# Kernel tuning notes

Hardware: AMD Instinct MI355X
Metric: run time of the kernel (lower is better)

## Reference

```python
import jax, jax.numpy as jnp
import numpy as np

NUM_HEADS = 16
NUM_KV_HEADS = 4
ROPE_THETA = 10000.0


def apply_rope(x, position_ids, theta):
    # x: [B, S, h, d]; position_ids: [B, S]
    d = x.shape[-1]
    freqs = 1.0 / theta ** (jnp.arange(0, d, 2, dtype=jnp.float32) / d)  # [d/2]
    angles = position_ids.astype(jnp.float32)[..., None] * freqs          # [B, S, d/2]
    cos = jnp.cos(angles)[:, :, None, :]                                  # [B, S, 1, d/2]
    sin = jnp.sin(angles)[:, :, None, :]
    xr = x.astype(jnp.float32).reshape(*x.shape[:-1], d // 2, 2)
    x0, x1 = xr[..., 0], xr[..., 1]
    o0 = x0 * cos - x1 * sin
    o1 = x0 * sin + x1 * cos
    out = jnp.stack((o0, o1), axis=-1).reshape(*x.shape)
    return out.astype(x.dtype)


def setup_inputs() -> dict:
    key = jax.random.key(0)
    k0, k1, k2, k3, k4 = jax.random.split(key, 5)
    B, S, H = 1, 2048, 2048
    Hkv = H // (NUM_HEADS // NUM_KV_HEADS)  # 512
    init_scale = 0.02 / np.sqrt(H)
    return {
        "hidden_states": jax.random.normal(k0, (B, S, H), jnp.float32),
        "attention_mask": jnp.ones((B, S), jnp.int32),
        "segment_ids": jnp.zeros((B, S), jnp.int32),
        "position_ids": jnp.broadcast_to(jnp.arange(S, dtype=jnp.int32)[None], (B, S)),
        "Wq": jax.random.normal(k1, (H, H), jnp.float32) * init_scale,
        "Wk": jax.random.normal(k2, (H, Hkv), jnp.float32) * init_scale,
        "Wv": jax.random.normal(k3, (H, Hkv), jnp.float32) * init_scale,
        "Wo": jax.random.normal(k4, (H, H), jnp.float32) * init_scale,
    }


def reference(hidden_states, attention_mask, segment_ids, position_ids, Wq, Wk, Wv, Wo):
    B, S, H = hidden_states.shape
    nh, nkv = NUM_HEADS, NUM_KV_HEADS
    g = nh // nkv
    hd = H // nh

    xq = (hidden_states @ Wq).reshape(B, S, nh, hd)
    xk = (hidden_states @ Wk).reshape(B, S, nkv, hd)
    xv = (hidden_states @ Wv).reshape(B, S, nkv, hd)
    # GQA repeat: 'b s (h d) -> b s (h g) d' == repeat each kv head g times contiguously
    xk = jnp.repeat(xk, g, axis=2)  # [B, S, nh, hd]
    xv = jnp.repeat(xv, g, axis=2)

    xq = apply_rope(xq, position_ids, ROPE_THETA)
    xk = apply_rope(xk, position_ids, ROPE_THETA)

    # masks: causal AND padding AND segment
    causal = jnp.tril(jnp.ones((S, S), dtype=bool))[None, None]            # [1,1,S,S]
    pad = (attention_mask > 0)[:, None, None, :]                            # [B,1,1,S]
    seg = (segment_ids[:, :, None] == segment_ids[:, None, :])[:, None]     # [B,1,S,S]
    mask = causal & pad & seg                                               # [B,1,S,S]

    scale = 1.0 / np.sqrt(hd)
    logits = jnp.einsum("bqhd,bkhd->bhqk", xq.astype(jnp.float32), xk.astype(jnp.float32)) * scale
    logits = jnp.where(mask, logits, jnp.finfo(jnp.float32).min)
    probs = jax.nn.softmax(logits, axis=-1).astype(xv.dtype)
    attn = jnp.einsum("bhqk,bkhd->bqhd", probs, xv)                         # [B,S,nh,hd]

    out = attn.reshape(B, S, H) @ Wo
    return out
```

## Files before the change

### kernel.cpp

```cpp
#include <hip/hip_runtime.h>
#include <hip/hip_bf16.h>
#include <stdint.h>
#include <math.h>

#define SS 2048
#define HH 2048
#define NH 16
#define NKV 4
#define HD 128
#define HKV 512
#define NQKV 3072

typedef __bf16 bf16x8 __attribute__((ext_vector_type(8)));
typedef float f32x4 __attribute__((ext_vector_type(4)));

static_assert(sizeof(bf16x8) == 16, "bf16x8 must be 16B");

__device__ __forceinline__ void async_ld16(const void* gp, void* lp) {
  __builtin_amdgcn_global_load_lds(
      (const __attribute__((address_space(1))) unsigned int*)(uintptr_t)gp,
      (__attribute__((address_space(3))) unsigned int*)(uintptr_t)lp,
      16, 0, 0);
}

__device__ __forceinline__ unsigned short f2bu(float f) {
  __hip_bfloat16 b = __float2bfloat16(f);
  return *reinterpret_cast<unsigned short*>(&b);
}

__global__ __launch_bounds__(256) void k_prep1(
    const float* __restrict__ X, const float* __restrict__ Wq, const float* __restrict__ Wk,
    const float* __restrict__ Wv, const float* __restrict__ Wo,
    const int* __restrict__ amv, const int* __restrict__ seg, int* __restrict__ kseg,
    float2* __restrict__ rtab,
    __hip_bfloat16* __restrict__ Xb, __hip_bfloat16* __restrict__ WqT,
    __hip_bfloat16* __restrict__ WkT, __hip_bfloat16* __restrict__ WvT,
    __hip_bfloat16* __restrict__ WoT) {
  __shared__ __align__(16) __hip_bfloat16 t2[64 * 72];
  int b = blockIdx.x;
  int t = threadIdx.y * 32 + threadIdx.x;
  if (b < 4096) {
    int i = b * 256 + t;
    float4 v = ((const float4*)X)[i];
    ushort4 o;
    o.x = f2bu(v.x); o.y = f2bu(v.y); o.z = f2bu(v.z); o.w = f2bu(v.w);
    ((ushort4*)Xb)[i] = o;
    return;
  }
  b -= 4096;
  if (b >= 2568) {
    int i = (b - 2568) * 256 + t;
    int p = i >> 6, f = i & 63;
    const float L2T_D64 = 0.20762050593046837f;
    float freq = exp2f(-L2T_D64 * (float)f);
    float sn, cs;
    sincosf((float)p * freq, &sn, &cs);
    rtab[i] = make_float2(sn, cs);
    return;
  }
  if (b >= 2560) {
    int i = (b - 2560) * 256 + t;
    kseg[i] = (amv[i] > 0) ? seg[i] : 0x7fffffff;
    return;
  }
  const float* src; __hip_bfloat16* dst; int xtiles;
  if (b < 1024)      { src = Wq; dst = WqT; xtiles = 32; }
  else if (b < 2048) { src = Wo; dst = WoT; xtiles = 32; b -= 1024; }
  else if (b < 2304) { src = Wk; dst = WkT; xtiles = 8;  b -= 2048; }
  else               { src = Wv; dst = WvT; xtiles = 8;  b -= 2304; }
  const int C = xtiles * 64;
  int bx = (b % xtiles) * 64;
  int by = (b / xtiles) * 64;
#pragma unroll
  for (int i = 0; i < 4; i++) {
    int idx = i * 256 + t;
    int r = idx >> 4, c4 = (idx & 15) * 4;
    float4 v = *(const float4*)(src + (size_t)(by + r) * C + bx + c4);
    t2[(c4 + 0) * 72 + r] = __float2bfloat16(v.x);
    t2[(c4 + 1) * 72 + r] = __float2bfloat16(v.y);
    t2[(c4 + 2) * 72 + r] = __float2bfloat16(v.z);
    t2[(c4 + 3) * 72 + r] = __float2bfloat16(v.w);
  }
  __syncthreads();
#pragma unroll
  for (int i = 0; i < 2; i++) {
    int idx = i * 256 + t;
    int rr = idx >> 3, cc = (idx & 7) * 8;
    *(bf16x8*)(dst + (size_t)(bx + rr) * HH + by + cc) =
        *(const bf16x8*)(&t2[rr * 72 + cc]);
  }
}

__global__ __launch_bounds__(256, 2) void k_gemm_qkv(
    const __hip_bfloat16* __restrict__ A, const __hip_bfloat16* __restrict__ B,
    __hip_bfloat16* __restrict__ Qb, __hip_bfloat16* __restrict__ Kb,
    __hip_bfloat16* __restrict__ Vt, const int* __restrict__ pos,
    const float2* __restrict__ rtab) {
  __shared__ __align__(16) __hip_bfloat16 sA0[64 * 64];
  __shared__ __align__(16) __hip_bfloat16 sA1[64 * 64];
  __shared__ __align__(16) __hip_bfloat16 sA2[64 * 64];
  __shared__ __align__(16) __hip_bfloat16 sB0[128 * 64];
  __shared__ __align__(16) __hip_bfloat16 sB1[128 * 64];
  __shared__ __align__(16) __hip_bfloat16 sB2[128 * 64];
  const int tid = threadIdx.x;
  const int lane = tid & 63;
  const int wave = tid >> 6;
  const int bm = blockIdx.y * 64;
  const int bn = blockIdx.x * 128;
  const int wm = (wave & 1) * 32;
  const int wn = (wave >> 1) * 64;
  const int am = lane & 15;
  const int ch = lane >> 4;

  f32x4 acc[2][4] = {};

  auto stage = [&](__hip_bfloat16* sA, __hip_bfloat16* sB, int k0) {
#pragma unroll
    for (int q = 0; q < 2; q++) {
      int c = q * 256 + tid;
      int row = c >> 3, kp = c & 7;
      int col = (kp ^ (row & 7)) * 8;
      async_ld16(A + (size_t)(bm + row) * HH + k0 + col, (char*)sA + c * 16);
    }
#pragma unroll
    for (int q = 0; q < 4; q++) {
      int c = q * 256 + tid;
      int row = c >> 3, kp = c & 7;
      int col = (kp ^ (row & 7)) * 8;
      async_ld16(B + (size_t)(bn + row) * HH + k0 + col, (char*)sB + c * 16);
    }
  };
  auto compute = [&](const __hip_bfloat16* sA, const __hip_bfloat16* sB) {
#pragma unroll
    for (int kb = 0; kb < 2; kb++) {
      bf16x8 a[2], b[4];
#pragma unroll
      for (int i = 0; i < 2; i++) {
        int row = wm + i * 16 + am;
        a[i] = *(const bf16x8*)(sA + row * 64 + (((kb * 4 + ch) ^ (row & 7)) * 8));
      }
#pragma unroll
      for (int j = 0; j < 4; j++) {
        int row = wn + j * 16 + am;
        b[j] = *(const bf16x8*)(sB + row * 64 + (((kb * 4 + ch) ^ (row & 7)) * 8));
      }
#pragma unroll
      for (int i = 0; i < 2; i++)
#pragma unroll
        for (int j = 0; j < 4; j++)
          acc[i][j] = __builtin_amdgcn_mfma_f32_16x16x32_bf16(a[i], b[j], acc[i][j], 0, 0, 0);
    }
  };

  __hip_bfloat16 *cA = sA0, *nA = sA1, *fA = sA2;
  __hip_bfloat16 *cB = sB0, *nB = sB1, *fB = sB2;
  stage(cA, cB, 0);
  stage(nA, nB, 64);
  for (int t = 0; t < 32; ++t) {
    if (t + 1 < 32) asm volatile("s_waitcnt vmcnt(6)" ::: "memory");
    else            asm volatile("s_waitcnt vmcnt(0)" ::: "memory");
    asm volatile("s_barrier" ::: "memory");
    if (t + 2 < 32) stage(fA, fB, (t + 2) * 64);
    compute(cA, cB);
    __hip_bfloat16* tp;
    tp = cA; cA = nA; nA = fA; fA = tp;
    tp = cB; cB = nB; nB = fB; fB = tp;
  }

  const bool isV = (bn >= HH + HKV);
  if (isV) {
#pragma unroll
    for (int j = 0; j < 4; j++) {
      int lc = bn + wn + j * 16 + am - (HH + HKV);
#pragma unroll
      for (int i = 0; i < 2; i++) {
        int row = bm + wm + i * 16 + ch * 4;
        ushort4 o;
        o.x = f2bu(acc[i][j][0]); o.y = f2bu(acc[i][j][1]);
        o.z = f2bu(acc[i][j][2]); o.w = f2bu(acc[i][j][3]);
        *(ushort4*)(Vt + (size_t)lc * SS + row) = o;
      }
    }
  } else {
    const float SCLQ = 0.08838834764831845f * 1.4426950408889634f;
    const bool isQ = (bn < HH);
    int pint[2][4];
#pragma unroll
    for (int i = 0; i < 2; i++)
#pragma unroll
      for (int r = 0; r < 4; r++)
        pint[i][r] = pos[bm + wm + i * 16 + ch * 4 + r];
    const float sgn = (am & 1) ? 1.0f : -1.0f;
#pragma unroll
    for (int j = 0; j < 4; j++) {
      int col = bn + wn + j * 16 + am;
      int lc = isQ ? col : (col - HH);
      int fidx = (lc >> 1) & 63;
#pragma unroll
      for (int i = 0; i < 2; i++)
#pragma unroll
        for (int r = 0; r < 4; r++) {
          float v = acc[i][j][r];
          float px = __shfl_xor(v, 1, 64);
          float2 sc = rtab[pint[i][r] * 64 + fidx];
          float o = v * sc.y + sgn * px * sc.x;
          int row = bm + wm + i * 16 + ch * 4 + r;
          if (isQ) Qb[(size_t)row * HH + col] = __float2bfloat16(o * SCLQ);
          else     Kb[(size_t)row * HKV + lc] = __float2bfloat16(o);
        }
    }
  }
}

__global__ __launch_bounds__(256, 3) void k_gemm_out(
    const __hip_bfloat16* __restrict__ A, const __hip_bfloat16* __restrict__ B,
    float* __restrict__ C) {
  __shared__ __align__(16) __hip_bfloat16 sA0[64 * 64];
  __shared__ __align__(16) __hip_bfloat16 sB0[128 * 64];
  __shared__ __align__(16) __hip_bfloat16 sA1[64 * 64];
  __shared__ __align__(16) __hip_bfloat16 sB1[128 * 64];
  const int tid = threadIdx.x;
  const int lane = tid & 63;
  const int wave = tid >> 6;
  const int bm = blockIdx.y * 64;
  const int bn = blockIdx.x * 128;
  const int wm = (wave & 1) * 32;
  const int wn = (wave >> 1) * 64;
  const int am = lane & 15;
  const int ch = lane >> 4;

  f32x4 acc[2][4] = {};

  auto stage = [&](__hip_bfloat16* sA, __hip_bfloat16* sB, int k0) {
#pragma unroll
    for (int q = 0; q < 2; q++) {
      int c = q * 256 + tid;
      int row = c >> 3, kp = c & 7;
      int col = (kp ^ (row & 7)) * 8;
      async_ld16(A + (size_t)(bm + row) * HH + k0 + col, (char*)sA + c * 16);
    }
#pragma unroll
    for (int q = 0; q < 4; q++) {
      int c = q * 256 + tid;
      int row = c >> 3, kp = c & 7;
      int col = (kp ^ (row & 7)) * 8;
      async_ld16(B + (size_t)(bn + row) * HH + k0 + col, (char*)sB + c * 16);
    }
  };
  auto compute = [&](const __hip_bfloat16* sA, const __hip_bfloat16* sB) {
#pragma unroll
    for (int kb = 0; kb < 2; kb++) {
      bf16x8 a[2], b[4];
#pragma unroll
      for (int i = 0; i < 2; i++) {
        int row = wm + i * 16 + am;
        a[i] = *(const bf16x8*)(sA + row * 64 + (((kb * 4 + ch) ^ (row & 7)) * 8));
      }
#pragma unroll
      for (int j = 0; j < 4; j++) {
        int row = wn + j * 16 + am;
        b[j] = *(const bf16x8*)(sB + row * 64 + (((kb * 4 + ch) ^ (row & 7)) * 8));
      }
#pragma unroll
      for (int i = 0; i < 2; i++)
#pragma unroll
        for (int j = 0; j < 4; j++)
          acc[i][j] = __builtin_amdgcn_mfma_f32_16x16x32_bf16(a[i], b[j], acc[i][j], 0, 0, 0);
    }
  };

  stage(sA0, sB0, 0);
  int k0 = 0;
  while (true) {
    __syncthreads();
    if (k0 + 64 < HH) stage(sA1, sB1, k0 + 64);
    compute(sA0, sB0);
    k0 += 64; if (k0 >= HH) break;
    __syncthreads();
    if (k0 + 64 < HH) stage(sA0, sB0, k0 + 64);
    compute(sA1, sB1);
    k0 += 64; if (k0 >= HH) break;
  }

#pragma unroll
  for (int i = 0; i < 2; i++)
#pragma unroll
    for (int j = 0; j < 4; j++)
#pragma unroll
      for (int r = 0; r < 4; r++) {
        int row = bm + wm + i * 16 + ch * 4 + r;
        int col = bn + wn + j * 16 + am;
        C[(size_t)row * HH + col] = acc[i][j][r];
      }
}

__global__ __launch_bounds__(256, 4) void k_attn(
    const __hip_bfloat16* __restrict__ Qb,
    const __hip_bfloat16* __restrict__ Kb,
    const __hip_bfloat16* __restrict__ Vt,
    const int* __restrict__ seg,
    const int* __restrict__ kseg,
    float* __restrict__ Obuf,
    float* __restrict__ Lbuf) {
  __shared__ __align__(16) __hip_bfloat16 sK[2][32 * 128];
  __shared__ __align__(16) __hip_bfloat16 sV[2][128 * 32];
  __shared__ __align__(16) __hip_bfloat16 sPall[4][16 * 32];

  const int bid = blockIdx.x;
  const int qt = 31 - (bid >> 5);
  const int h = (bid >> 1) & 15;
  const int half = bid & 1;
  const int T = 2 * (qt + 1);
  const int n0 = qt + 1;
  const int kt0 = half ? n0 : 0;
  const int kt1 = half ? T : n0;

  const int kvh = h >> 2;
  const int tid = threadIdx.x, lane = tid & 63, w = tid >> 6;
  const int am = lane & 15, ch = lane >> 4;
  const int qrow0 = qt * 64 + w * 16;
  char* sP = (char*)&sPall[w][0];

  bf16x8 qf[4];
#pragma unroll
  for (int ks = 0; ks < 4; ks++)
    qf[ks] = *(const bf16x8*)(Qb + (size_t)(qrow0 + am) * HH + h * HD + ks * 32 + ch * 8);

  int segq[4];
#pragma unroll
  for (int r = 0; r < 4; r++) segq[r] = seg[qrow0 + ch * 4 + r];
  const int q0 = seg[qrow0];
  const bool quni = __all((segq[0] == q0) && (segq[1] == q0) &&
                          (segq[2] == q0) && (segq[3] == q0));

  f32x4 o_acc[8] = {};
  float l_s[4] = {0.f, 0.f, 0.f, 0.f};

  auto stage = [&](int kt, int p) {
#pragma unroll
    for (int q = 0; q < 2; q++) {
      int c = q * 256 + tid;
      int row = c >> 4, kp = c & 15;
      int col = (kp ^ (row & 15)) * 8;
      async_ld16(Kb + (size_t)(kt * 32 + row) * HKV + kvh * 128 + col, (char*)sK[p] + c * 16);
    }
#pragma unroll
    for (int q = 0; q < 2; q++) {
      int c = q * 256 + tid;
      int row = c >> 2, kp = c & 3;
      int col = (kp ^ ((row >> 1) & 3)) * 8;
      async_ld16(Vt + (size_t)(kvh * 128 + row) * SS + kt * 32 + col, (char*)sV[p] + c * 16);
    }
  };

  stage(kt0, 0);
  for (int kt = kt0; kt < kt1; kt++) {
    const int p = (kt - kt0) & 1;
    const int kbase = kt * 32;
    const bool skip = (kbase > qrow0 + 15);
    __syncthreads();

    int kinfo[2];
    if (!skip) {
#pragma unroll
      for (int jt = 0; jt < 2; jt++) kinfo[jt] = kseg[kbase + jt * 16 + am];
    }
    if (kt + 1 < kt1) stage(kt + 1, p ^ 1);
    if (!skip) {
      f32x4 sacc[2] = {};
      __builtin_amdgcn_s_setprio(1);
#pragma unroll
      for (int ks = 0; ks < 4; ks++)
#pragma unroll
        for (int jt = 0; jt < 2; jt++) {
          bf16x8 kf = *(const bf16x8*)(sK[p] + (jt * 16 + am) * 128 + (((ks * 4 + ch) ^ am) * 8));
          sacc[jt] = __builtin_amdgcn_mfma_f32_16x16x32_bf16(qf[ks], kf, sacc[jt], 0, 0, 0);
        }
      __builtin_amdgcn_s_setprio(0);

      const bool needc = (kbase + 31 > qrow0);
      const bool fast = quni && !needc &&
          __all((kinfo[0] == q0) && (kinfo[1] == q0));

      if (fast) {
#pragma unroll
        for (int jt = 0; jt < 2; jt++)
#pragma unroll
          for (int r = 0; r < 4; r++) {
            float pv = exp2f(sacc[jt][r] - 8.0f);
            l_s[r] += pv;
            int row = ch * 4 + r;
            int chunk = (jt * 2 + (am >> 3)) ^ (row & 3);
            *(__hip_bfloat16*)(sP + row * 64 + chunk * 16 + (am & 7) * 2) =
                __float2bfloat16(pv);
          }
      } else {
#pragma unroll
        for (int jt = 0; jt < 2; jt++) {
          int kk = kbase + jt * 16 + am;
#pragma unroll
          for (int r = 0; r < 4; r++) {
            int qrow = qrow0 + ch * 4 + r;
            bool ok = (kinfo[jt] == segq[r]) && (kk <= qrow);
            float pv = ok ? exp2f(sacc[jt][r] - 8.0f) : 0.0f;
            l_s[r] += pv;
            int row = ch * 4 + r;
            int chunk = (jt * 2 + (am >> 3)) ^ (row & 3);
            *(__hip_bfloat16*)(sP + row * 64 + chunk * 16 + (am & 7) * 2) =
                __float2bfloat16(pv);
          }
        }
      }

      __builtin_amdgcn_s_setprio(1);
      {
        bf16x8 pf = *(const bf16x8*)(sP + am * 64 + ((ch ^ (am & 3)) * 16));
#pragma unroll
        for (int jt = 0; jt < 8; jt++) {
          int vrow = jt * 16 + am;
          bf16x8 vf = *(const bf16x8*)(sV[p] + vrow * 32 + ((ch ^ ((vrow >> 1) & 3)) * 8));
          o_acc[jt] = __builtin_amdgcn_mfma_f32_16x16x32_bf16(pf, vf, o_acc[jt], 0, 0, 0);
        }
      }
      __builtin_amdgcn_s_setprio(0);
    }
  }

#pragma unroll
  for (int off = 1; off < 16; off <<= 1)
#pragma unroll
    for (int r = 0; r < 4; r++) l_s[r] += __shfl_xor(l_s[r], off, 64);
  if (am == 0)
#pragma unroll
    for (int r = 0; r < 4; r++)
      unsafeAtomicAdd(Lbuf + (size_t)(qrow0 + ch * 4 + r) * NH + h, l_s[r]);
#pragma unroll
  for (int jt = 0; jt < 8; jt++)
#pragma unroll
    for (int r = 0; r < 4; r++) {
      int row = qrow0 + ch * 4 + r;
      unsafeAtomicAdd(Obuf + (size_t)row * HH + h * HD + jt * 16 + am, o_acc[jt][r]);
    }
}

__global__ __launch_bounds__(256) void k_norm(
    const float* __restrict__ Obuf, const float* __restrict__ Lbuf,
    __hip_bfloat16* __restrict__ Ab) {
  int i = blockIdx.x * 256 + threadIdx.x;
  int s = i >> 9;
  int hIdx = (i & 511) >> 5;
  float inv = 1.0f / Lbuf[(size_t)s * NH + hIdx];
  float4 v = ((const float4*)Obuf)[i];
  ushort4 o;
  o.x = f2bu(v.x * inv); o.y = f2bu(v.y * inv);
  o.z = f2bu(v.z * inv); o.w = f2bu(v.w * inv);
  ((ushort4*)Ab)[i] = o;
}

extern "C" void kernel_launch(void* const* d_in, const int* in_sizes, int n_in,
                              void* d_out, int out_size, void* d_ws, size_t ws_size,
                              hipStream_t stream) {
  const float* X  = (const float*)d_in[0];
  const int* amv  = (const int*)d_in[1];
  const int* seg  = (const int*)d_in[2];
  const int* pos  = (const int*)d_in[3];
  const float* Wq = (const float*)d_in[4];
  const float* Wk = (const float*)d_in[5];
  const float* Wv = (const float*)d_in[6];
  const float* Wo = (const float*)d_in[7];
  float* out = (float*)d_out;

  char* ws = (char*)d_ws;
  size_t off = 0;
  auto alloc = [&](size_t bytes) { void* p = ws + off; off += (bytes + 255) & ~(size_t)255; return p; };
  __hip_bfloat16* Xb   = (__hip_bfloat16*)alloc((size_t)SS * HH * 2);
  __hip_bfloat16* WqT  = (__hip_bfloat16*)alloc((size_t)HH * HH * 2);
  __hip_bfloat16* WkT  = (__hip_bfloat16*)alloc((size_t)HKV * HH * 2);
  __hip_bfloat16* WvT  = (__hip_bfloat16*)alloc((size_t)HKV * HH * 2);
  __hip_bfloat16* WoT  = (__hip_bfloat16*)alloc((size_t)HH * HH * 2);
  __hip_bfloat16* Qb   = (__hip_bfloat16*)alloc((size_t)SS * HH * 2);
  __hip_bfloat16* Kb   = (__hip_bfloat16*)alloc((size_t)SS * HKV * 2);
  __hip_bfloat16* Vt   = (__hip_bfloat16*)alloc((size_t)HKV * SS * 2);
  __hip_bfloat16* Ab   = (__hip_bfloat16*)alloc((size_t)SS * HH * 2);
  float*          Obuf = (float*)alloc((size_t)SS * HH * 4);
  float*          Lbuf = (float*)alloc((size_t)SS * NH * 4);
  int*            kseg = (int*)alloc((size_t)SS * 4);
  float2*         rtab = (float2*)alloc((size_t)SS * 64 * 8);
  (void)WkT; (void)WvT;

  hipMemsetAsync(Obuf, 0, (size_t)SS * HH * 4 + ((size_t)SS * NH * 4 + 255 & ~(size_t)255), stream);
  k_prep1<<<dim3(7176), dim3(32, 8), 0, stream>>>(X, Wq, Wk, Wv, Wo, amv, seg, kseg, rtab,
                                                  Xb, WqT, WkT, WvT, WoT);
  k_gemm_qkv<<<dim3(NQKV / 128, SS / 64), 256, 0, stream>>>(Xb, WqT, Qb, Kb, Vt, pos, rtab);
  k_attn<<<dim3(1024), 256, 0, stream>>>(Qb, Kb, Vt, seg, kseg, Obuf, Lbuf);
  k_norm<<<dim3(SS * HH / 4 / 256), 256, 0, stream>>>(Obuf, Lbuf, Ab);
  k_gemm_out<<<dim3(HH / 128, SS / 64), 256, 0, stream>>>(Ab, WoT, out);
}
```

Before: 234.0 us.

## Retile QKV GEMM to 128x96 blocks with swizzled 512-block grid and double buffering

Changes the fused QKV projection GEMM from 64x128 tiles over a 24x32 grid to 128x96 tiles over a flat 512-block grid. Block indices are remapped so neighbouring blocks share A/B panels in cache. The triple-buffered async LDS pipeline becomes a double buffer with an extra barrier per iteration. Each wave now computes a 64x48 sub-tile (4x3 MFMA tiles), raising register use and arithmetic per LDS load. The epilogue now decides per 16-column group whether output goes to Q, K, or V, because a 96-wide tile can cross the Q/K/V boundaries.

```diff
diff --git a/kernel.cpp b/kernel.cpp
--- a/kernel.cpp
+++ b/kernel.cpp
@@ -96,108 +96,103 @@
     __hip_bfloat16* __restrict__ Qb, __hip_bfloat16* __restrict__ Kb,
     __hip_bfloat16* __restrict__ Vt, const int* __restrict__ pos,
     const float2* __restrict__ rtab) {
-  __shared__ __align__(16) __hip_bfloat16 sA0[64 * 64];
-  __shared__ __align__(16) __hip_bfloat16 sA1[64 * 64];
-  __shared__ __align__(16) __hip_bfloat16 sA2[64 * 64];
-  __shared__ __align__(16) __hip_bfloat16 sB0[128 * 64];
-  __shared__ __align__(16) __hip_bfloat16 sB1[128 * 64];
-  __shared__ __align__(16) __hip_bfloat16 sB2[128 * 64];
+  __shared__ __align__(16) __hip_bfloat16 sA[2][128 * 64];
+  __shared__ __align__(16) __hip_bfloat16 sB[2][96 * 64];
   const int tid = threadIdx.x;
   const int lane = tid & 63;
   const int wave = tid >> 6;
-  const int bm = blockIdx.y * 64;
-  const int bn = blockIdx.x * 128;
-  const int wm = (wave & 1) * 32;
-  const int wn = (wave >> 1) * 64;
+  const int lid = blockIdx.x;
+  const int swz = (lid & 7) * 64 + (lid >> 3);
+  const int bm = (swz >> 5) * 128;
+  const int bn = (swz & 31) * 96;
+  const int wm = (wave & 1) * 64;
+  const int wn = (wave >> 1) * 48;
   const int am = lane & 15;
   const int ch = lane >> 4;
 
-  f32x4 acc[2][4] = {};
-
-  auto stage = [&](__hip_bfloat16* sA, __hip_bfloat16* sB, int k0) {
-#pragma unroll
-    for (int q = 0; q < 2; q++) {
+  f32x4 acc[4][3] = {};
+
+  auto stage = [&](int p, int k0) {
+#pragma unroll
+    for (int q = 0; q < 4; q++) {
       int c = q * 256 + tid;
       int row = c >> 3, kp = c & 7;
       int col = (kp ^ (row & 7)) * 8;
-      async_ld16(A + (size_t)(bm + row) * HH + k0 + col, (char*)sA + c * 16);
-    }
-#pragma unroll
-    for (int q = 0; q < 4; q++) {
+      async_ld16(A + (size_t)(bm + row) * HH + k0 + col, (char*)&sA[p][0] + c * 16);
+    }
+#pragma unroll
+    for (int q = 0; q < 3; q++) {
       int c = q * 256 + tid;
       int row = c >> 3, kp = c & 7;
       int col = (kp ^ (row & 7)) * 8;
-      async_ld16(B + (size_t)(bn + row) * HH + k0 + col, (char*)sB + c * 16);
+      async_ld16(B + (size_t)(bn + row) * HH + k0 + col, (char*)&sB[p][0] + c * 16);
     }
   };
-  auto compute = [&](const __hip_bfloat16* sA, const __hip_bfloat16* sB) {
+  auto compute = [&](int p) {
 #pragma unroll
     for (int kb = 0; kb < 2; kb++) {
-      bf16x8 a[2], b[4];
-#pragma unroll
-      for (int i = 0; i < 2; i++) {
+      bf16x8 a[4], b[3];
+#pragma unroll
+      for (int i = 0; i < 4; i++) {
         int row = wm + i * 16 + am;
-        a[i] = *(const bf16x8*)(sA + row * 64 + (((kb * 4 + ch) ^ (row & 7)) * 8));
-      }
-#pragma unroll
-      for (int j = 0; j < 4; j++) {
+        a[i] = *(const bf16x8*)(&sA[p][0] + row * 64 + (((kb * 4 + ch) ^ (row & 7)) * 8));
+      }
+#pragma unroll
+      for (int j = 0; j < 3; j++) {
         int row = wn + j * 16 + am;
-        b[j] = *(const bf16x8*)(sB + row * 64 + (((kb * 4 + ch) ^ (row & 7)) * 8));
-      }
-#pragma unroll
-      for (int i = 0; i < 2; i++)
-#pragma unroll
-        for (int j = 0; j < 4; j++)
+        b[j] = *(const bf16x8*)(&sB[p][0] + row * 64 + (((kb * 4 + ch) ^ (row & 7)) * 8));
+      }
+#pragma unroll
+      for (int i = 0; i < 4; i++)
+#pragma unroll
+        for (int j = 0; j < 3; j++)
           acc[i][j] = __builtin_amdgcn_mfma_f32_16x16x32_bf16(a[i], b[j], acc[i][j], 0, 0, 0);
     }
   };
 
-  __hip_bfloat16 *cA = sA0, *nA = sA1, *fA = sA2;
-  __hip_bfloat16 *cB = sB0, *nB = sB1, *fB = sB2;
-  stage(cA, cB, 0);
-  stage(nA, nB, 64);
+  stage(0, 0);
+  int cur = 0;
   for (int t = 0; t < 32; ++t) {
-    if (t + 1 < 32) asm volatile("s_waitcnt vmcnt(6)" ::: "memory");
-    else            asm volatile("s_waitcnt vmcnt(0)" ::: "memory");
+    if (t + 1 < 32) {
+      stage(cur ^ 1, (t + 1) * 64);
+      asm volatile("s_waitcnt vmcnt(7)" ::: "memory");
+    } else {
+      asm volatile("s_waitcnt vmcnt(0)" ::: "memory");
+    }
     asm volatile("s_barrier" ::: "memory");
-    if (t + 2 < 32) stage(fA, fB, (t + 2) * 64);
-    compute(cA, cB);
-    __hip_bfloat16* tp;
-    tp = cA; cA = nA; nA = fA; fA = tp;
-    tp = cB; cB = nB; nB = fB; fB = tp;
-  }
-
-  const bool isV = (bn >= HH + HKV);
-  if (isV) {
-#pragma unroll
-    for (int j = 0; j < 4; j++) {
-      int lc = bn + wn + j * 16 + am - (HH + HKV);
-#pragma unroll
-      for (int i = 0; i < 2; i++) {
+    compute(cur);
+    asm volatile("s_barrier" ::: "memory");
+    cur ^= 1;
+  }
+
+  const float SCLQ = 0.08838834764831845f * 1.4426950408889634f;
+  const float sgn = (am & 1) ? 1.0f : -1.0f;
+  int pint[4][4];
+#pragma unroll
+  for (int i = 0; i < 4; i++)
+#pragma unroll
+    for (int r = 0; r < 4; r++)
+      pint[i][r] = pos[bm + wm + i * 16 + ch * 4 + r];
+#pragma unroll
+  for (int j = 0; j < 3; j++) {
+    const int colbase = bn + wn + j * 16;
+    const int col = colbase + am;
+    if (colbase >= HH + HKV) {
+      int lc = col - (HH + HKV);
+#pragma unroll
+      for (int i = 0; i < 4; i++) {
         int row = bm + wm + i * 16 + ch * 4;
         ushort4 o;
         o.x = f2bu(acc[i][j][0]); o.y = f2bu(acc[i][j][1]);
         o.z = f2bu(acc[i][j][2]); o.w = f2bu(acc[i][j][3]);
         *(ushort4*)(Vt + (size_t)lc * SS + row) = o;
       }
-    }
-  } else {
-    const float SCLQ = 0.08838834764831845f * 1.4426950408889634f;
-    const bool isQ = (bn < HH);
-    int pint[2][4];
-#pragma unroll
-    for (int i = 0; i < 2; i++)
-#pragma unroll
-      for (int r = 0; r < 4; r++)
-        pint[i][r] = pos[bm + wm + i * 16 + ch * 4 + r];
-    const float sgn = (am & 1) ? 1.0f : -1.0f;
-#pragma unroll
-    for (int j = 0; j < 4; j++) {
-      int col = bn + wn + j * 16 + am;
+    } else {
+      const bool isQ = (colbase < HH);
       int lc = isQ ? col : (col - HH);
       int fidx = (lc >> 1) & 63;
 #pragma unroll
-      for (int i = 0; i < 2; i++)
+      for (int i = 0; i < 4; i++)
 #pragma unroll
         for (int r = 0; r < 4; r++) {
           float v = acc[i][j][r];
@@ -491,7 +486,7 @@
   hipMemsetAsync(Obuf, 0, (size_t)SS * HH * 4 + ((size_t)SS * NH * 4 + 255 & ~(size_t)255), stream);
   k_prep1<<<dim3(7176), dim3(32, 8), 0, stream>>>(X, Wq, Wk, Wv, Wo, amv, seg, kseg, rtab,
                                                   Xb, WqT, WkT, WvT, WoT);
-  k_gemm_qkv<<<dim3(NQKV / 128, SS / 64), 256, 0, stream>>>(Xb, WqT, Qb, Kb, Vt, pos, rtab);
+  k_gemm_qkv<<<dim3(512), 256, 0, stream>>>(Xb, WqT, Qb, Kb, Vt, pos, rtab);
   k_attn<<<dim3(1024), 256, 0, stream>>>(Qb, Kb, Vt, seg, kseg, Obuf, Lbuf);
   k_norm<<<dim3(SS * HH / 4 / 256), 256, 0, stream>>>(Obuf, Lbuf, Ab);
   k_gemm_out<<<dim3(HH / 128, SS / 64), 256, 0, stream>>>(Ab, WoT, out);
```

Measured after the change: 222.7 us. 4.8% less time.
